# Kernel optimization log

Measured on AMD Instinct MI355X. Metric: run time of the kernel, lower is better.

## Reference

```python
import jax, jax.numpy as jnp
import numpy as np

H_IN, W_IN = 128, 128  # sensor grid; region=(1,1), stride=(1,1) -> one RF per pixel


def setup_inputs() -> dict:
    key = jax.random.key(0)
    k1, k2, k3, k4, k5, k6 = jax.random.split(key, 6)
    B, N, C, HID = 8, 2048, 16, 128
    s = 1.0 / np.sqrt(HID)
    features = jax.random.normal(k1, (B, N, C), dtype=jnp.float32)
    coords = jax.random.randint(k2, (B, N, 2), 0, 128, dtype=jnp.int32)  # (x, y)
    w_ih = jax.random.normal(k3, (4 * HID, C), dtype=jnp.float32) * s
    w_hh = jax.random.normal(k4, (4 * HID, HID), dtype=jnp.float32) * s
    b_ih = jax.random.normal(k5, (4 * HID,), dtype=jnp.float32) * s
    b_hh = jax.random.normal(k6, (4 * HID,), dtype=jnp.float32) * s
    return {"features": features, "coords": coords, "w_ih": w_ih,
            "w_hh": w_hh, "b_ih": b_ih, "b_hh": b_hh}


def reference(features, coords, w_ih, w_hh, b_ih, b_hh):
    """MatrixLSTM with 1x1 non-overlapping receptive fields.

    Events (time-ordered along axis 1) are routed to their pixel's RF; a shared
    LSTM is run over each RF's event sequence and the last output per RF is
    scattered into a dense [B, hidden, H, W] map (zeros where no events).
    Implemented as one lax.scan over events with per-RF (h, c) state.
    """
    B, N, C = features.shape
    HID = w_hh.shape[1]
    # coord2idx: raster order y * W + x  -> RF id per event, [B, N]
    rf = coords[:, :, 1].astype(jnp.int32) * W_IN + coords[:, :, 0].astype(jnp.int32)
    bidx = jnp.arange(B)
    bias = b_ih + b_hh

    def step(carry, inp):
        h_all, c_all = carry              # [B, num_rf, HID] each
        x_t, rf_t = inp                   # [B, C], [B]
        h_prev = h_all[bidx, rf_t]        # gather per-RF state, [B, HID]
        c_prev = c_all[bidx, rf_t]
        gates = x_t @ w_ih.T + h_prev @ w_hh.T + bias  # [B, 4*HID]
        i, f, g, o = jnp.split(gates, 4, axis=-1)       # torch LSTM gate order
        i = jax.nn.sigmoid(i)
        f = jax.nn.sigmoid(f)
        g = jnp.tanh(g)
        o = jax.nn.sigmoid(o)
        c_new = f * c_prev + i * g
        h_new = o * jnp.tanh(c_new)
        h_all = h_all.at[bidx, rf_t].set(h_new)        # scatter back
        c_all = c_all.at[bidx, rf_t].set(c_new)
        return (h_all, c_all), None

    h0 = jnp.zeros((B, H_IN * W_IN, HID), features.dtype)
    c0 = jnp.zeros_like(h0)
    (h_all, _), _ = jax.lax.scan(step, (h0, c0),
                                 (features.transpose(1, 0, 2), rf.T))
    # final h per RF == LSTM output at each RF's last event; zeros if no events
    return h_all.reshape(B, H_IN, W_IN, HID).transpose(0, 3, 1, 2)
```

## Files before the change

### kernel.cpp

```cpp
#include <hip/hip_runtime.h>
#include <hip/hip_bf16.h>
#include <math.h>

#define B 8
#define N 2048
#define C 16
#define HID 128
#define NRF 16384
#define MAXLEN 8
#define MAXCH 2048

__device__ __forceinline__ float sigf(float x) { return 1.f / (1.f + expf(-x)); }

__global__ __launch_bounds__(1024) void k_pre(
    const int* __restrict__ coords, const float* __restrict__ w_ih,
    const float* __restrict__ w_hh, const float* __restrict__ b_ih,
    const float* __restrict__ b_hh, float* __restrict__ w_ih_T,
    float* __restrict__ w_hh_T, float* __restrict__ biassum,
    int* __restrict__ map, int* __restrict__ cnt, int* __restrict__ mcnt,
    int* __restrict__ chainpk, int* __restrict__ mlist,
    int* __restrict__ slots) {
    int tid = threadIdx.x;
    if (blockIdx.x < 8) {
        int bb = blockIdx.x;
        __shared__ int cnt_l[NRF];
        __shared__ int nch_l, nmul_l;
#pragma unroll
        for (int i = 0; i < 16; i++) cnt_l[tid + 1024 * i] = 0;
        if (tid == 0) { nch_l = 0; nmul_l = 0; }
#pragma unroll
        for (int i = 0; i < 16; i++) map[bb * NRF + tid + 1024 * i] = -1;
        __syncthreads();
        int n0 = tid, n1 = tid + 1024;
        int2 c0 = ((const int2*)coords)[bb * N + n0];
        int2 c1 = ((const int2*)coords)[bb * N + n1];
        int rf0 = c0.y * 128 + c0.x;
        int rf1 = c1.y * 128 + c1.x;
        int pos0 = atomicAdd(&cnt_l[rf0], 1);
        int pos1 = atomicAdd(&cnt_l[rf1], 1);
        if (pos0 < MAXLEN) slots[((size_t)bb * NRF + rf0) * MAXLEN + pos0] = n0;
        if (pos1 < MAXLEN) slots[((size_t)bb * NRF + rf1) * MAXLEN + pos1] = n1;
        __syncthreads();
#pragma unroll
        for (int e = 0; e < 2; e++) {
            int rf = e ? rf1 : rf0;
            int pos = e ? pos1 : pos0;
            if (pos == 0) {
                int j = atomicAdd(&nch_l, 1);
                int len = cnt_l[rf];
                if (len > MAXLEN) len = MAXLEN;
                map[bb * NRF + rf] = j;
                int* sl = slots + ((size_t)bb * NRF + rf) * MAXLEN;
                int ev[MAXLEN];
#pragma unroll
                for (int t = 0; t < MAXLEN; t++) {
                    int v = sl[t];
                    ev[t] = (t < len) ? v : 0x7fffffff;
                }
#pragma unroll
                for (int a = 0; a < MAXLEN; a++)
#pragma unroll
                    for (int q = 0; q < MAXLEN - 1; q++) {
                        int u = ev[q], v = ev[q + 1];
                        ev[q] = min(u, v);
                        ev[q + 1] = max(u, v);
                    }
                if (len >= 2) {
                    for (int t = 0; t < len; t++) sl[t] = ev[t];
                    int m = atomicAdd(&nmul_l, 1);
                    if (m < 1024) mlist[bb * 1024 + m] = j | (rf << 11);
                }
                chainpk[bb * MAXCH + j] = ev[0] | (len << 11);
            }
        }
        __syncthreads();
        if (tid == 0) {
            cnt[bb] = nch_l;
            mcnt[bb] = (nmul_l > 1024) ? 1024 : nmul_l;
        }
    } else {
        int i = (blockIdx.x - 8) * 1024 + tid;
        if (i < C * 512) {
            int c = i >> 9, j = i & 511;
            w_ih_T[i] = w_ih[j * C + c];
        }
        if (i < HID * 512) {
            int k = i >> 9, j = i & 511;
            w_hh_T[i] = w_hh[j * HID + k];
        }
        if (i < 512) biassum[i] = b_ih[i] + b_hh[i];
    }
}

__global__ __launch_bounds__(256) void k_gate0(
    const float* __restrict__ features, const float* __restrict__ w_ih_T,
    const float* __restrict__ biassum, const int* __restrict__ cnt,
    const int* __restrict__ chainpk, float* __restrict__ hfin,
    float* __restrict__ cfin) {
    int tid = threadIdx.x;
    int bb = blockIdx.x >> 7;
    int slot0 = (blockIdx.x & 127) * 16;
    __shared__ float ls_w[C * 512];
    __shared__ float ls_b[512];
    __shared__ int l_pk[16];
    int nc = cnt[bb];
    if (tid < 16) {
        int j = slot0 + tid;
        l_pk[tid] = (j < nc) ? chainpk[bb * MAXCH + j] : -1;
    }
    for (int i = tid; i < C * 128; i += 256)
        ((float4*)ls_w)[i] = ((const float4*)w_ih_T)[i];
    ls_b[tid] = biassum[tid];
    ls_b[tid + 256] = biassum[tid + 256];
    __syncthreads();
    int w = tid >> 6, lane = tid & 63;
    int pk[4];
    float f[4];
#pragma unroll
    for (int s2 = 0; s2 < 4; s2++) {
        pk[s2] = l_pk[w * 4 + s2];
        f[s2] = 0.f;
        if (pk[s2] >= 0 && lane < 16)
            f[s2] = features[((size_t)(bb * N + (pk[s2] & 2047))) * C + lane];
    }
#pragma unroll
    for (int s2 = 0; s2 < 4; s2++) {
        if (pk[s2] < 0) continue;
        int len = pk[s2] >> 11;
        float ai0 = ls_b[lane],       ai1 = ls_b[lane + 64];
        float ag0 = ls_b[lane + 256], ag1 = ls_b[lane + 320];
        float ao0 = ls_b[lane + 384], ao1 = ls_b[lane + 448];
#pragma unroll
        for (int c2 = 0; c2 < 16; c2++) {
            float xv = __shfl(f[s2], c2, 64);
            ai0 += ls_w[c2 * 512 + lane]       * xv;
            ai1 += ls_w[c2 * 512 + lane + 64]  * xv;
            ag0 += ls_w[c2 * 512 + lane + 256] * xv;
            ag1 += ls_w[c2 * 512 + lane + 320] * xv;
            ao0 += ls_w[c2 * 512 + lane + 384] * xv;
            ao1 += ls_w[c2 * 512 + lane + 448] * xv;
        }
        float c0 = sigf(ai0) * tanhf(ag0);
        float c1 = sigf(ai1) * tanhf(ag1);
        float h0 = sigf(ao0) * tanhf(c0);
        float h1 = sigf(ao1) * tanhf(c1);
        size_t idx = (size_t)(bb * MAXCH + slot0 + w * 4 + s2);
        hfin[idx * HID + lane] = h0;
        hfin[idx * HID + lane + 64] = h1;
        if (len >= 2) {
            cfin[idx * HID + lane] = c0;
            cfin[idx * HID + lane + 64] = c1;
        }
    }
}

__global__ __launch_bounds__(256) void k_recur(
    const float* __restrict__ features, const float* __restrict__ w_ih_T,
    const float* __restrict__ w_hh_T, const float* __restrict__ biassum,
    const int* __restrict__ chainpk, const int* __restrict__ mcnt,
    const int* __restrict__ mlist, const int* __restrict__ slots,
    float* __restrict__ hfin, const float* __restrict__ cfin) {
    int tid = threadIdx.x;
    int bb = blockIdx.x >> 7;
    int m0 = blockIdx.x & 127;
    int M = mcnt[bb];
    if (m0 >= M) return;
    __shared__ float h_s[HID], c_s[HID];
    __shared__ float x_s[16];
    __shared__ float g_s[512];
    float bs0 = biassum[tid], bs1 = biassum[tid + 256];
    for (int m = m0; m < M; m += 128) {
        int e = mlist[bb * 1024 + m];
        int j = e & 2047;
        int rf = e >> 11;
        size_t idx = (size_t)(bb * MAXCH + j);
        int len = chainpk[bb * MAXCH + j] >> 11;
        const int* sl = slots + ((size_t)bb * NRF + rf) * MAXLEN;
        if (tid < 16) x_s[tid] = features[((size_t)(bb * N + sl[1])) * C + tid];
        if (tid < 128) {
            h_s[tid] = hfin[idx * HID + tid];
            c_s[tid] = cfin[idx * HID + tid];
        }
        __syncthreads();
        for (int t = 1; t < len; t++) {
            float a0 = bs0, a1 = bs1, b0 = 0.f, b1 = 0.f;
#pragma unroll
            for (int c2 = 0; c2 < 16; c2++) {
                float xv = x_s[c2];
                a0 += w_ih_T[c2 * 512 + tid] * xv;
                a1 += w_ih_T[c2 * 512 + tid + 256] * xv;
            }
#pragma unroll 8
            for (int k = 0; k < 128; k += 2) {
                float h0 = h_s[k], h1 = h_s[k + 1];
                a0 += w_hh_T[k * 512 + tid] * h0;
                a1 += w_hh_T[k * 512 + tid + 256] * h0;
                b0 += w_hh_T[(k + 1) * 512 + tid] * h1;
                b1 += w_hh_T[(k + 1) * 512 + tid + 256] * h1;
            }
            g_s[tid] = a0 + b0;
            g_s[tid + 256] = a1 + b1;
            __syncthreads();
            if (tid < 128) {
                float ig = sigf(g_s[tid]);
                float fg = sigf(g_s[tid + 128]);
                float gg = tanhf(g_s[tid + 256]);
                float og = sigf(g_s[tid + 384]);
                float cn = fg * c_s[tid] + ig * gg;
                c_s[tid] = cn;
                h_s[tid] = og * tanhf(cn);
            }
            if (tid < 16 && t + 1 < len)
                x_s[tid] = features[((size_t)(bb * N + sl[t + 1])) * C + tid];
            __syncthreads();
        }
        if (tid < 128) hfin[idx * HID + tid] = h_s[tid];
        __syncthreads();
    }
}

__global__ __launch_bounds__(256) void k_scatter(
    const float* __restrict__ hfin, const int* __restrict__ map,
    float* __restrict__ out) {
    int b = blockIdx.x >> 7;
    int y = blockIdx.x & 127;
    int t = threadIdx.x;
    int xq = t & 31;
    int hg = t >> 5;
    const int4* mrow = (const int4*)(map + b * NRF + y * 128);
    int4 kk = mrow[xq];
    const float* hb = hfin + (size_t)b * MAXCH * HID;
#pragma unroll
    for (int hh = 0; hh < 16; hh++) {
        int hid = hg * 16 + hh;
        float4 v;
        v.x = (kk.x < 0) ? 0.f : hb[kk.x * HID + hid];
        v.y = (kk.y < 0) ? 0.f : hb[kk.y * HID + hid];
        v.z = (kk.z < 0) ? 0.f : hb[kk.z * HID + hid];
        v.w = (kk.w < 0) ? 0.f : hb[kk.w * HID + hid];
        *(float4*)(out + ((((size_t)b * HID + hid) * 128 + y) * 128) + xq * 4) = v;
    }
}

extern "C" void kernel_launch(void* const* d_in, const int* in_sizes, int n_in,
                              void* d_out, int out_size, void* d_ws, size_t ws_size,
                              hipStream_t stream) {
    const float* features = (const float*)d_in[0];
    const int*   coords   = (const int*)d_in[1];
    const float* w_ih     = (const float*)d_in[2];
    const float* w_hh     = (const float*)d_in[3];
    const float* b_ih     = (const float*)d_in[4];
    const float* b_hh     = (const float*)d_in[5];
    float* out = (float*)d_out;

    char* ws = (char*)d_ws;
    float* w_ih_T   = (float*)(ws + 0);
    float* w_hh_T   = (float*)(ws + 32768);
    float* biassum  = (float*)(ws + 294912);
    int*   map      = (int*)(ws + 296960);
    int*   cnt      = (int*)(ws + 821248);
    int*   mcnt     = (int*)(ws + 821312);
    int*   chainpk  = (int*)(ws + 821376);
    int*   mlist    = (int*)(ws + 886912);
    int*   slots    = (int*)(ws + 919680);
    float* hfin     = (float*)(ws + 5113984);
    float* cfin     = (float*)(ws + 13502592);

    k_pre<<<dim3(81), dim3(1024), 0, stream>>>(
        coords, w_ih, w_hh, b_ih, b_hh, w_ih_T, w_hh_T, biassum,
        map, cnt, mcnt, chainpk, mlist, slots);
    k_gate0<<<dim3(1024), dim3(256), 0, stream>>>(
        features, w_ih_T, biassum, cnt, chainpk, hfin, cfin);
    k_recur<<<dim3(1024), dim3(256), 0, stream>>>(
        features, w_ih_T, w_hh_T, biassum, chainpk, mcnt, mlist, slots,
        hfin, cfin);
    k_scatter<<<dim3(B * 128), dim3(256), 0, stream>>>(hfin, map, out);
}
```

Baseline: 138.3 us.

## Fuse first-step gate and recurrence kernels into one launch with role-split blocks

Merges k_gate0 and k_recur into a single 512-thread kernel. The first 1024 blocks run full chains (length ≥2) starting from zero state, with w_ih columns held in registers. The remaining blocks handle only single-event chains. This removes one launch, the cfin buffer, and the hfin/cfin round trip between kernels. The cost is that multi-event chains now compute their first step inside the serial recurrence loop, and the larger blocks may change occupancy.

```diff
diff --git a/kernel.cpp b/kernel.cpp
--- a/kernel.cpp
+++ b/kernel.cpp
@@ -92,130 +92,114 @@
     }
 }
 
-__global__ __launch_bounds__(256) void k_gate0(
+__global__ __launch_bounds__(512) void k_main(
     const float* __restrict__ features, const float* __restrict__ w_ih_T,
-    const float* __restrict__ biassum, const int* __restrict__ cnt,
-    const int* __restrict__ chainpk, float* __restrict__ hfin,
-    float* __restrict__ cfin) {
+    const float* __restrict__ w_hh_T, const float* __restrict__ biassum,
+    const int* __restrict__ cnt, const int* __restrict__ chainpk,
+    const int* __restrict__ mcnt, const int* __restrict__ mlist,
+    const int* __restrict__ slots, float* __restrict__ hfin) {
     int tid = threadIdx.x;
-    int bb = blockIdx.x >> 7;
-    int slot0 = (blockIdx.x & 127) * 16;
     __shared__ float ls_w[C * 512];
     __shared__ float ls_b[512];
     __shared__ int l_pk[16];
-    int nc = cnt[bb];
-    if (tid < 16) {
-        int j = slot0 + tid;
-        l_pk[tid] = (j < nc) ? chainpk[bb * MAXCH + j] : -1;
-    }
-    for (int i = tid; i < C * 128; i += 256)
-        ((float4*)ls_w)[i] = ((const float4*)w_ih_T)[i];
-    ls_b[tid] = biassum[tid];
-    ls_b[tid + 256] = biassum[tid + 256];
-    __syncthreads();
-    int w = tid >> 6, lane = tid & 63;
-    int pk[4];
-    float f[4];
-#pragma unroll
-    for (int s2 = 0; s2 < 4; s2++) {
-        pk[s2] = l_pk[w * 4 + s2];
-        f[s2] = 0.f;
-        if (pk[s2] >= 0 && lane < 16)
-            f[s2] = features[((size_t)(bb * N + (pk[s2] & 2047))) * C + lane];
-    }
-#pragma unroll
-    for (int s2 = 0; s2 < 4; s2++) {
-        if (pk[s2] < 0) continue;
-        int len = pk[s2] >> 11;
-        float ai0 = ls_b[lane],       ai1 = ls_b[lane + 64];
-        float ag0 = ls_b[lane + 256], ag1 = ls_b[lane + 320];
-        float ao0 = ls_b[lane + 384], ao1 = ls_b[lane + 448];
-#pragma unroll
-        for (int c2 = 0; c2 < 16; c2++) {
-            float xv = __shfl(f[s2], c2, 64);
-            ai0 += ls_w[c2 * 512 + lane]       * xv;
-            ai1 += ls_w[c2 * 512 + lane + 64]  * xv;
-            ag0 += ls_w[c2 * 512 + lane + 256] * xv;
-            ag1 += ls_w[c2 * 512 + lane + 320] * xv;
-            ao0 += ls_w[c2 * 512 + lane + 384] * xv;
-            ao1 += ls_w[c2 * 512 + lane + 448] * xv;
-        }
-        float c0 = sigf(ai0) * tanhf(ag0);
-        float c1 = sigf(ai1) * tanhf(ag1);
-        float h0 = sigf(ao0) * tanhf(c0);
-        float h1 = sigf(ao1) * tanhf(c1);
-        size_t idx = (size_t)(bb * MAXCH + slot0 + w * 4 + s2);
-        hfin[idx * HID + lane] = h0;
-        hfin[idx * HID + lane + 64] = h1;
-        if (len >= 2) {
-            cfin[idx * HID + lane] = c0;
-            cfin[idx * HID + lane + 64] = c1;
-        }
-    }
-}
-
-__global__ __launch_bounds__(256) void k_recur(
-    const float* __restrict__ features, const float* __restrict__ w_ih_T,
-    const float* __restrict__ w_hh_T, const float* __restrict__ biassum,
-    const int* __restrict__ chainpk, const int* __restrict__ mcnt,
-    const int* __restrict__ mlist, const int* __restrict__ slots,
-    float* __restrict__ hfin, const float* __restrict__ cfin) {
-    int tid = threadIdx.x;
-    int bb = blockIdx.x >> 7;
-    int m0 = blockIdx.x & 127;
-    int M = mcnt[bb];
-    if (m0 >= M) return;
-    __shared__ float h_s[HID], c_s[HID];
-    __shared__ float x_s[16];
-    __shared__ float g_s[512];
-    float bs0 = biassum[tid], bs1 = biassum[tid + 256];
-    for (int m = m0; m < M; m += 128) {
-        int e = mlist[bb * 1024 + m];
-        int j = e & 2047;
-        int rf = e >> 11;
-        size_t idx = (size_t)(bb * MAXCH + j);
-        int len = chainpk[bb * MAXCH + j] >> 11;
-        const int* sl = slots + ((size_t)bb * NRF + rf) * MAXLEN;
-        if (tid < 16) x_s[tid] = features[((size_t)(bb * N + sl[1])) * C + tid];
-        if (tid < 128) {
-            h_s[tid] = hfin[idx * HID + tid];
-            c_s[tid] = cfin[idx * HID + tid];
-        }
-        __syncthreads();
-        for (int t = 1; t < len; t++) {
-            float a0 = bs0, a1 = bs1, b0 = 0.f, b1 = 0.f;
+    __shared__ float h_s[HID], c_s[HID], x_s[16], g_s[512];
+
+    if (blockIdx.x < 1024) {
+        int bb = blockIdx.x >> 7;
+        int m0 = blockIdx.x & 127;
+        int M = mcnt[bb];
+        if (m0 >= M) return;
+        float wi[16];
+#pragma unroll
+        for (int c2 = 0; c2 < 16; c2++) wi[c2] = w_ih_T[c2 * 512 + tid];
+        float bs = biassum[tid];
+        for (int m = m0; m < M; m += 128) {
+            int e = mlist[bb * 1024 + m];
+            int j = e & 2047, rf = e >> 11;
+            size_t idx = (size_t)(bb * MAXCH + j);
+            int len = chainpk[bb * MAXCH + j] >> 11;
+            const int* sl = slots + ((size_t)bb * NRF + rf) * MAXLEN;
+            if (tid < 16) x_s[tid] = features[((size_t)(bb * N + sl[0])) * C + tid];
+            if (tid < 128) c_s[tid] = 0.f;
+            __syncthreads();
+            for (int t = 0; t < len; t++) {
+                float a0 = bs, a1 = 0.f, a2 = 0.f, a3 = 0.f;
+#pragma unroll
+                for (int c2 = 0; c2 < 16; c2++) a0 += wi[c2] * x_s[c2];
+                if (t > 0) {
+#pragma unroll 8
+                    for (int k = 0; k < 128; k += 4) {
+                        a0 += w_hh_T[k * 512 + tid]       * h_s[k];
+                        a1 += w_hh_T[(k + 1) * 512 + tid] * h_s[k + 1];
+                        a2 += w_hh_T[(k + 2) * 512 + tid] * h_s[k + 2];
+                        a3 += w_hh_T[(k + 3) * 512 + tid] * h_s[k + 3];
+                    }
+                }
+                g_s[tid] = (a0 + a1) + (a2 + a3);
+                __syncthreads();
+                if (tid < 128) {
+                    float ig = sigf(g_s[tid]);
+                    float fg = sigf(g_s[tid + 128]);
+                    float gg = tanhf(g_s[tid + 256]);
+                    float og = sigf(g_s[tid + 384]);
+                    float cn = fg * c_s[tid] + ig * gg;
+                    c_s[tid] = cn;
+                    h_s[tid] = og * tanhf(cn);
+                }
+                if (tid < 16 && t + 1 < len)
+                    x_s[tid] = features[((size_t)(bb * N + sl[t + 1])) * C + tid];
+                __syncthreads();
+            }
+            if (tid < 128) hfin[idx * HID + tid] = h_s[tid];
+            __syncthreads();
+        }
+    } else {
+        int b2 = blockIdx.x - 1024;
+        int bb = b2 >> 7;
+        int slot0 = (b2 & 127) * 16;
+        int nc = cnt[bb];
+        if (tid < 16) {
+            int j = slot0 + tid;
+            l_pk[tid] = (j < nc) ? chainpk[bb * MAXCH + j] : -1;
+        }
+        for (int i = tid; i < C * 128; i += 512)
+            ((float4*)ls_w)[i] = ((const float4*)w_ih_T)[i];
+        ls_b[tid] = biassum[tid];
+        __syncthreads();
+        int w = tid >> 6, lane = tid & 63;
+        int pk[2];
+        float f[2];
+#pragma unroll
+        for (int s2 = 0; s2 < 2; s2++) {
+            pk[s2] = l_pk[w * 2 + s2];
+            f[s2] = 0.f;
+            if (pk[s2] >= 0 && (pk[s2] >> 11) == 1 && lane < 16)
+                f[s2] = features[((size_t)(bb * N + (pk[s2] & 2047))) * C + lane];
+        }
+#pragma unroll
+        for (int s2 = 0; s2 < 2; s2++) {
+            if (pk[s2] < 0 || (pk[s2] >> 11) != 1) continue;
+            float ai0 = ls_b[lane],       ai1 = ls_b[lane + 64];
+            float ag0 = ls_b[lane + 256], ag1 = ls_b[lane + 320];
+            float ao0 = ls_b[lane + 384], ao1 = ls_b[lane + 448];
 #pragma unroll
             for (int c2 = 0; c2 < 16; c2++) {
-                float xv = x_s[c2];
-                a0 += w_ih_T[c2 * 512 + tid] * xv;
-                a1 += w_ih_T[c2 * 512 + tid + 256] * xv;
+                float xv = __shfl(f[s2], c2, 64);
+                ai0 += ls_w[c2 * 512 + lane]       * xv;
+                ai1 += ls_w[c2 * 512 + lane + 64]  * xv;
+                ag0 += ls_w[c2 * 512 + lane + 256] * xv;
+                ag1 += ls_w[c2 * 512 + lane + 320] * xv;
+                ao0 += ls_w[c2 * 512 + lane + 384] * xv;
+                ao1 += ls_w[c2 * 512 + lane + 448] * xv;
             }
-#pragma unroll 8
-            for (int k = 0; k < 128; k += 2) {
-                float h0 = h_s[k], h1 = h_s[k + 1];
-                a0 += w_hh_T[k * 512 + tid] * h0;
-                a1 += w_hh_T[k * 512 + tid + 256] * h0;
-                b0 += w_hh_T[(k + 1) * 512 + tid] * h1;
-                b1 += w_hh_T[(k + 1) * 512 + tid + 256] * h1;
-            }
-            g_s[tid] = a0 + b0;
-            g_s[tid + 256] = a1 + b1;
-            __syncthreads();
-            if (tid < 128) {
-                float ig = sigf(g_s[tid]);
-                float fg = sigf(g_s[tid + 128]);
-                float gg = tanhf(g_s[tid + 256]);
-                float og = sigf(g_s[tid + 384]);
-                float cn = fg * c_s[tid] + ig * gg;
-                c_s[tid] = cn;
-                h_s[tid] = og * tanhf(cn);
-            }
-            if (tid < 16 && t + 1 < len)
-                x_s[tid] = features[((size_t)(bb * N + sl[t + 1])) * C + tid];
-            __syncthreads();
-        }
-        if (tid < 128) hfin[idx * HID + tid] = h_s[tid];
-        __syncthreads();
+            float c0 = sigf(ai0) * tanhf(ag0);
+            float c1 = sigf(ai1) * tanhf(ag1);
+            float h0 = sigf(ao0) * tanhf(c0);
+            float h1 = sigf(ao1) * tanhf(c1);
+            size_t idx = (size_t)(bb * MAXCH + slot0 + w * 2 + s2);
+            hfin[idx * HID + lane] = h0;
+            hfin[idx * HID + lane + 64] = h1;
+        }
     }
 }
 
@@ -264,15 +248,12 @@
     int*   mlist    = (int*)(ws + 886912);
     int*   slots    = (int*)(ws + 919680);
     float* hfin     = (float*)(ws + 5113984);
-    float* cfin     = (float*)(ws + 13502592);
 
     k_pre<<<dim3(81), dim3(1024), 0, stream>>>(
         coords, w_ih, w_hh, b_ih, b_hh, w_ih_T, w_hh_T, biassum,
         map, cnt, mcnt, chainpk, mlist, slots);
-    k_gate0<<<dim3(1024), dim3(256), 0, stream>>>(
-        features, w_ih_T, biassum, cnt, chainpk, hfin, cfin);
-    k_recur<<<dim3(1024), dim3(256), 0, stream>>>(
-        features, w_ih_T, w_hh_T, biassum, chainpk, mcnt, mlist, slots,
-        hfin, cfin);
+    k_main<<<dim3(2048), dim3(512), 0, stream>>>(
+        features, w_ih_T, w_hh_T, biassum, cnt, chainpk, mcnt, mlist,
+        slots, hfin);
     k_scatter<<<dim3(B * 128), dim3(256), 0, stream>>>(hfin, map, out);
 }
```

Measured after the change: 128.5 us. 1.08x faster.
